# Kernel optimization log

Hardware: AMD Instinct MI355X
Metric: run time of the kernel (lower is better)

The kernel has to match this reference:

```python
import jax, jax.numpy as jnp
import numpy as np

B, N, D = 512, 100000, 64
TAU = 1e-4            # gumbel-softmax temperature from source
SIM_RATIO = 0.5       # similarity_ratio init kwarg
COS_EPS = 1e-6


def setup_inputs() -> dict:
    key = jax.random.key(0)
    k1, k2, k3, k4, k5 = jax.random.split(key, 5)
    need_replace = jax.random.randint(k1, (B, 2), 0, N, dtype=jnp.int64) if jax.config.jax_enable_x64 else jax.random.randint(k1, (B, 2), 0, N, dtype=jnp.int32)
    union_feature = jax.random.normal(k2, (B, 2 * D), dtype=jnp.float32)
    all_items = jax.random.normal(k3, (N, D), dtype=jnp.float32) * 0.1
    W = jax.random.normal(k4, (D, 2 * D), dtype=jnp.float32) * 0.05
    b = jax.random.normal(k5, (D,), dtype=jnp.float32) * 0.01
    return {"need_replace": need_replace, "union_feature": union_feature,
            "all_items": all_items, "W": W, "b": b}


def _cosine(a, b):
    # torch.nn.CosineSimilarity(dim=1, eps=1e-6): dot / max(||a||*||b||, eps)
    dot = jnp.sum(a * b, axis=1)
    na = jnp.linalg.norm(a, axis=1)
    nb = jnp.linalg.norm(b, axis=1)
    return dot / jnp.maximum(na * nb, COS_EPS)


def reference(need_replace, union_feature, all_items, W, b):
    item_ids = need_replace[:, 1]
    items_emb = all_items[item_ids]                      # [B, D]
    uif = union_feature @ W.T + b                        # [B, D] (nn.Linear)
    score = uif @ all_items.T                            # [B, N]

    # gumbel_softmax(tau=1e-4, hard=True), training branch
    g = jax.random.gumbel(jax.random.key(42), score.shape, dtype=score.dtype)
    y_soft = jax.nn.softmax((score + g) / TAU, axis=-1)  # [B, N]
    idx = jnp.argmax(y_soft, axis=-1)                    # [B]
    y_hard = jax.nn.one_hot(idx, N, dtype=score.dtype)
    P = y_hard + y_soft - jax.lax.stop_gradient(y_soft)  # straight-through hard one-hot

    item_sequence = jnp.arange(N, dtype=score.dtype)[None, :]
    replaceable_items = jnp.sum(P * item_sequence, axis=-1).astype(jnp.int32)
    replaceable_feat = P @ all_items                     # [B, D]

    sim = _cosine(items_emb, replaceable_feat)
    sim = (sim + 1.0) / 2.0                              # regularize_similarity
    labels = jnp.full((B,), SIM_RATIO, dtype=sim.dtype)
    similarity_loss = jnp.mean((sim - labels) ** 2)      # SimilarityMarginLoss (assumed MSE-to-margin)
    return replaceable_items, replaceable_feat, similarity_loss, jnp.mean(sim)
```

## Files before the change

### kernel.cpp

```cpp
#include <hip/hip_runtime.h>
#include <cstdint>

#define NITEMS   100000
#define BROWS    512
#define DDIM     64
#define S_BLOCKS 391
#define AM4_N    (S_BLOCKS * 4)
#define SB_OUT   256
#define NTILES   3125
#define FB_X     64
#define FB_Y     8
#define FB_CHUNK 1568
#define OUT_FEAT 512
#define OUT_LOSS (512 + 512 * 64)
#define OUT_MSIM (OUT_LOSS + 1)

#define BITS_RAW_T 4284334592u
#define G_TE       6.001f

typedef __attribute__((ext_vector_type(8)))  short  bf16x8;
typedef __attribute__((ext_vector_type(16))) float  f32x16;
typedef unsigned long long u64;
typedef uint32_t u32;

#define ROTL(x, r) __builtin_amdgcn_alignbit((x), (x), 32u - (r))

__device__ __forceinline__ u32 threefry_0_42_xor(u32 e) {
    const u32 K1 = 42u;
    const u32 K2 = 0x1BD11BDAu ^ 42u;
    u32 x0 = 0u;
    u32 x1 = e + K1;
#define TFR(r) { x0 += x1; x1 = ROTL(x1, r) ^ x0; }
    TFR(13u) TFR(15u) TFR(26u) TFR(6u)
    x0 += K1;  x1 += K2 + 1u;
    TFR(17u) TFR(29u) TFR(16u) TFR(24u)
    x0 += K2;  x1 += 2u;
    TFR(13u) TFR(15u) TFR(26u) TFR(6u)
    x1 += K1 + 3u;
    TFR(17u) TFR(29u) TFR(16u) TFR(24u)
    x0 += K1;  x1 += K2 + 4u;
    TFR(13u) TFR(15u) TFR(26u) TFR(6u)
    x0 += K2;  x1 += 5u;
#undef TFR
    return x0 ^ x1;
}

__device__ __forceinline__ void threefry_quad(u32 e0, u32 e1, u32 e2, u32 e3,
                                              u32& r0, u32& r1, u32& r2, u32& r3) {
    const u32 K1 = 42u;
    const u32 K2 = 0x1BD11BDAu ^ 42u;
    u32 a0 = 0u, a1 = e0 + K1;
    u32 b0 = 0u, b1 = e1 + K1;
    u32 c0 = 0u, c1 = e2 + K1;
    u32 d0 = 0u, d1 = e3 + K1;
#define TFR4(r) { a0 += a1; b0 += b1; c0 += c1; d0 += d1; \
                  a1 = ROTL(a1, r) ^ a0; b1 = ROTL(b1, r) ^ b0; \
                  c1 = ROTL(c1, r) ^ c0; d1 = ROTL(d1, r) ^ d0; }
    TFR4(13u) TFR4(15u) TFR4(26u) TFR4(6u)
    a0 += K1; a1 += K2 + 1u;  b0 += K1; b1 += K2 + 1u;
    c0 += K1; c1 += K2 + 1u;  d0 += K1; d1 += K2 + 1u;
    TFR4(17u) TFR4(29u) TFR4(16u) TFR4(24u)
    a0 += K2; a1 += 2u;       b0 += K2; b1 += 2u;
    c0 += K2; c1 += 2u;       d0 += K2; d1 += 2u;
    TFR4(13u) TFR4(15u) TFR4(26u) TFR4(6u)
    a1 += K1 + 3u;            b1 += K1 + 3u;
    c1 += K1 + 3u;            d1 += K1 + 3u;
    TFR4(17u) TFR4(29u) TFR4(16u) TFR4(24u)
    a0 += K1; a1 += K2 + 4u;  b0 += K1; b1 += K2 + 4u;
    c0 += K1; c1 += K2 + 4u;  d0 += K1; d1 += K2 + 4u;
    TFR4(13u) TFR4(15u) TFR4(26u) TFR4(6u)
    a0 += K2; a1 += 5u;       b0 += K2; b1 += 5u;
    c0 += K2; c1 += 5u;       d0 += K2; d1 += 5u;
#undef TFR4
    r0 = a0 ^ a1; r1 = b0 ^ b1; r2 = c0 ^ c1; r3 = d0 ^ d1;
}

__device__ __forceinline__ float gumbel_from_bits(u32 b) {
    float f = __uint_as_float((b >> 9) | 0x3F800000u) - 1.0f;
    f = fmaxf(f, 1.17549435e-38f);
    return -logf(-logf(f));
}
__device__ __forceinline__ u32 order_map(float v) {
    u32 x = __float_as_uint(v);
    return (x & 0x80000000u) ? ~x : (x | 0x80000000u);
}
__device__ __forceinline__ float unpack_val(u64 p) {
    u32 x = (u32)(p >> 32);
    u32 f = (x & 0x80000000u) ? (x & 0x7FFFFFFFu) : ~x;
    return __uint_as_float(f);
}
__device__ __forceinline__ short f32_to_bf16_rne(float f) {
    u32 b = __float_as_uint(f);
    u32 r = (b + 0x7FFFu + ((b >> 16) & 1u)) >> 16;
    return (short)r;
}
__device__ __forceinline__ float bf16_to_f32(short h) {
    return __uint_as_float(((u32)(uint16_t)h) << 16);
}

__global__ void prep_kernel(const float* __restrict__ UF, const float* __restrict__ W,
                            const float* __restrict__ bias, const float* __restrict__ A,
                            float* __restrict__ uif, float* __restrict__ unorm,
                            float* __restrict__ wsAM4, int* __restrict__ cnt,
                            int* __restrict__ done, float* __restrict__ out) {
    const int t = threadIdx.x, b = blockIdx.x;
    if (b == 0) {
        if (t == 0) { *cnt = 0; out[OUT_LOSS] = 0.f; out[OUT_MSIM] = 0.f; }
        done[t] = 0; done[t + 256] = 0;
    }
    if (b < 128) {
        __shared__ float Wt[128 * 65];
        for (int i = t; i < 8192; i += 256) {
            int d = i >> 7, k = i & 127;
            Wt[k * 65 + d] = W[i];
        }
        __syncthreads();
        const int row = b * 4 + (t >> 6);
        const int d   = t & 63;
        const float* u = UF + row * 128;
        float s = 0.f;
#pragma unroll 4
        for (int k = 0; k < 128; k++) s = fmaf(u[k], Wt[k * 65 + d], s);
        s += bias[d];
        uif[row * 64 + d] = s;
        float q = s * s;
#pragma unroll
        for (int o = 32; o >= 1; o >>= 1) q += __shfl_xor(q, o);
        if (d == 0) unorm[row] = sqrtf(q);
    } else {
        const int item = (b - 128) * 256 + t;
        float q = 0.f;
        if (item < NITEMS) {
            const float4* r = (const float4*)(A + (size_t)item * DDIM);
#pragma unroll
            for (int k = 0; k < 16; k++) {
                float4 x = r[k];
                q = fmaf(x.x, x.x, q); q = fmaf(x.y, x.y, q);
                q = fmaf(x.z, x.z, q); q = fmaf(x.w, x.w, q);
            }
        }
        float n = sqrtf(q);
#pragma unroll
        for (int o = 32; o >= 1; o >>= 1) n = fmaxf(n, __shfl_xor(n, o));
        if ((t & 63) == 0) wsAM4[(b - 128) * 4 + (t >> 6)] = n;
    }
}

__global__ __launch_bounds__(256, 6) void phase1_kernel(
        const float* __restrict__ A, const float* __restrict__ uif,
        u64* __restrict__ wsT1, float* __restrict__ wsB) {
    __shared__ bf16x8 sh_ah[4 * 64];
    __shared__ bf16x8 sh_al[4 * 64];
    const int tid  = threadIdx.x;
    const int lane = tid & 63;
    const int wv   = tid >> 6;
    const int rg   = blockIdx.y;
    const int xb   = blockIdx.x;
    const int row   = rg * 128 + wv * 32 + (lane & 31);
    const int khalf = (lane >> 5) * 8;

    bf16x8 uh[4], ul[4];
#pragma unroll
    for (int s = 0; s < 4; s++) {
        const float* src = uif + row * 64 + khalf + 16 * s;
        float4 v0 = *(const float4*)src;
        float4 v1 = *(const float4*)(src + 4);
        float vv[8] = {v0.x, v0.y, v0.z, v0.w, v1.x, v1.y, v1.z, v1.w};
        bf16x8 h, l2;
#pragma unroll
        for (int j = 0; j < 8; j++) {
            short hh = f32_to_bf16_rne(vv[j]);
            float r  = vv[j] - bf16_to_f32(hh);
            h[j] = hh; l2[j] = f32_to_bf16_rne(r);
        }
        uh[s] = h; ul[s] = l2;
    }

    u64 t1p = 0ull; float t1f = -3.0e38f, t2f = -3.0e38f, sm = -3.0e38f;
    const u32 rowbase_e = (u32)row * (u32)NITEMS;

    const int s_i   = tid & 31;
    const int s_c   = tid >> 5;
    const int s_dst = (s_c >> 1) * 64 + s_i + 32 * (s_c & 1);
    const float* s_srcbase = A + (size_t)s_i * 64 + 8 * s_c;

    int t_idx = xb;
    float4 p0 = *(const float4*)(s_srcbase + (size_t)t_idx * (32 * 64));
    float4 p1 = *(const float4*)(s_srcbase + (size_t)t_idx * (32 * 64) + 4);

    while (t_idx < NTILES) {
        const int tb = t_idx * 32;
        bf16x8 h, l2;
        {
            float vv[8] = {p0.x, p0.y, p0.z, p0.w, p1.x, p1.y, p1.z, p1.w};
#pragma unroll
            for (int j = 0; j < 8; j++) {
                short hh = f32_to_bf16_rne(vv[j]);
                float r  = vv[j] - bf16_to_f32(hh);
                h[j] = hh; l2[j] = f32_to_bf16_rne(r);
            }
        }
        __syncthreads();
        sh_ah[s_dst] = h; sh_al[s_dst] = l2;
        __syncthreads();
        t_idx += SB_OUT;
        if (t_idx < NTILES) {
            const float* src = s_srcbase + (size_t)t_idx * (32 * 64);
            p0 = *(const float4*)src;
            p1 = *(const float4*)(src + 4);
        }

        f32x16 acc;
#pragma unroll
        for (int z = 0; z < 16; z++) acc[z] = 0.0f;
#pragma unroll
        for (int s = 0; s < 4; s++) {
            bf16x8 ah = sh_ah[s * 64 + lane];
            bf16x8 al = sh_al[s * 64 + lane];
            acc = __builtin_amdgcn_mfma_f32_32x32x16_bf16(ah, uh[s], acc, 0, 0, 0);
            acc = __builtin_amdgcn_mfma_f32_32x32x16_bf16(al, uh[s], acc, 0, 0, 0);
            acc = __builtin_amdgcn_mfma_f32_32x32x16_bf16(ah, ul[s], acc, 0, 0, 0);
        }

        const int ib4 = tb + 4 * (lane >> 5);
#pragma unroll
        for (int i = 0; i < 16; i += 4) {
            const int i0 = ib4 + 2 * i;
            u32 r0, r1, r2, r3;
            threefry_quad(rowbase_e + (u32)(i0 + 0), rowbase_e + (u32)(i0 + 1),
                          rowbase_e + (u32)(i0 + 2), rowbase_e + (u32)(i0 + 3),
                          r0, r1, r2, r3);
            float sA = acc[i], sB = acc[i + 1], sC = acc[i + 2], sD = acc[i + 3];
            sm = fmaxf(sm, fmaxf(fmaxf(sA, sB), fmaxf(sC, sD)));
            if (r0 >= BITS_RAW_T) {
                float v = sA + gumbel_from_bits(r0);
                if (v > t1f) {
                    t2f = t1f; t1f = v;
                    t1p = ((u64)order_map(v) << 32) | (u32)(~(u32)(i0 + 0));
                } else t2f = fmaxf(t2f, v);
            }
            if (r1 >= BITS_RAW_T) {
                float v = sB + gumbel_from_bits(r1);
                if (v > t1f) {
                    t2f = t1f; t1f = v;
                    t1p = ((u64)order_map(v) << 32) | (u32)(~(u32)(i0 + 1));
                } else t2f = fmaxf(t2f, v);
            }
            if (r2 >= BITS_RAW_T) {
                float v = sC + gumbel_from_bits(r2);
                if (v > t1f) {
                    t2f = t1f; t1f = v;
                    t1p = ((u64)order_map(v) << 32) | (u32)(~(u32)(i0 + 2));
                } else t2f = fmaxf(t2f, v);
            }
            if (r3 >= BITS_RAW_T) {
                float v = sD + gumbel_from_bits(r3);
                if (v > t1f) {
                    t2f = t1f; t1f = v;
                    t1p = ((u64)order_map(v) << 32) | (u32)(~(u32)(i0 + 3));
                } else t2f = fmaxf(t2f, v);
            }
        }
    }

    float bnd = fmaxf(t2f, sm + G_TE);
    {
        u64   op = __shfl_xor(t1p, 32);
        float of = __shfl_xor(t1f, 32);
        float ob = __shfl_xor(bnd, 32);
        if (op > t1p) { bnd = fmaxf(fmaxf(bnd, ob), t1f); t1p = op; t1f = of; }
        else          { bnd = fmaxf(fmaxf(bnd, ob), of); }
    }
    if (lane < 32) {
        wsT1[(size_t)row * SB_OUT + xb] = t1p;
        wsB [(size_t)row * SB_OUT + xb] = bnd;
    }
}

__global__ void merge_kernel(const u64* __restrict__ wsT1, const float* __restrict__ wsB,
                             const float* __restrict__ wsAM4, const float* __restrict__ unorm,
                             const float* __restrict__ A, const int* __restrict__ need_replace,
                             u64* __restrict__ packed, int* __restrict__ rowlist,
                             int* __restrict__ cnt, float* __restrict__ out) {
    const int row = blockIdx.x, t = threadIdx.x;
    float am = 0.f;
    for (int i = t; i < AM4_N; i += 64) am = fmaxf(am, wsAM4[i]);
    u64 p1 = 0ull; float f1 = -3.0e38f, f2 = -3.0e38f;
    for (int sbk = t; sbk < SB_OUT; sbk += 64) {
        u64   ep = wsT1[(size_t)row * SB_OUT + sbk];
        float e2 = wsB [(size_t)row * SB_OUT + sbk];
        if (ep > p1) { f2 = fmaxf(fmaxf(f1, e2), f2); p1 = ep; f1 = unpack_val(ep); }
        else         { float v = unpack_val(ep); f2 = fmaxf(f2, fmaxf(v, e2)); }
    }
#pragma unroll
    for (int off = 1; off < 64; off <<= 1) {
        u64   op  = __shfl_xor(p1, off);
        float of1 = __shfl_xor(f1, off);
        float of2 = __shfl_xor(f2, off);
        am = fmaxf(am, __shfl_xor(am, off));
        if (op > p1) { f2 = fmaxf(fmaxf(f1, of2), f2); p1 = op; f1 = of1; }
        else         { f2 = fmaxf(f2, fmaxf(of1, of2)); }
    }
    const float E = 1.5e-4f * unorm[row] * am + 3.0e-5f;
    if (f1 - f2 > 2.0f * E) {
        const int idx = (int)(~(u32)(p1 & 0xFFFFFFFFull));
        float fr = A[(size_t)idx * DDIM + t];
        out[OUT_FEAT + row * DDIM + t] = fr;
        int   item = need_replace[2 * row + 1];
        float fa   = A[(size_t)item * DDIM + t];
        float dot = fa * fr, na2 = fa * fa, nb2 = fr * fr;
#pragma unroll
        for (int o = 32; o >= 1; o >>= 1) {
            dot += __shfl_down(dot, o);
            na2 += __shfl_down(na2, o);
            nb2 += __shfl_down(nb2, o);
        }
        if (t == 0) {
            out[row] = (float)idx;
            float denom = fmaxf(sqrtf(na2) * sqrtf(nb2), 1e-6f);
            float sim = (dot / denom + 1.0f) * 0.5f;
            float d = sim - 0.5f;
            atomicAdd(&out[OUT_LOSS], d * d * (1.0f / 512.0f));
            atomicAdd(&out[OUT_MSIM], sim * (1.0f / 512.0f));
        }
    } else if (t == 0) {
        packed[row] = 0ull;
        rowlist[atomicAdd(cnt, 1)] = row;
    }
}

__global__ void fallback_kernel(const float* __restrict__ A, const float* __restrict__ uif,
                                const int* __restrict__ rowlist, const int* __restrict__ cnt,
                                const int* __restrict__ need_replace,
                                u64* __restrict__ packed, int* __restrict__ done,
                                float* __restrict__ out) {
    __shared__ float Us[64];
    __shared__ int   sh_last;
    const int t  = threadIdx.x;
    const int xb = blockIdx.x;
    const int total = *cnt;
    const int iend = min((xb + 1) * FB_CHUNK, NITEMS);

    for (int li = blockIdx.y; li < total; li += FB_Y) {
        const int row = rowlist[li];
        __syncthreads();
        if (t < 64) Us[t] = uif[row * 64 + t];
        __syncthreads();
        u64 pk = 0ull;
        for (int item = xb * FB_CHUNK + t; item < iend; item += 256) {
            u32 rb  = threefry_0_42_xor((u32)row * (u32)NITEMS + (u32)item);
            float g = gumbel_from_bits(rb);
            const float4* a4 = (const float4*)(A + (size_t)item * DDIM);
            float s0 = 0.f, s1 = 0.f;
#pragma unroll
            for (int k = 0; k < 16; k += 2) {
                float4 x = a4[k];
                float4 y = a4[k + 1];
                s0 = fmaf(x.x, Us[4*k    ], s0);
                s0 = fmaf(x.y, Us[4*k + 1], s0);
                s0 = fmaf(x.z, Us[4*k + 2], s0);
                s0 = fmaf(x.w, Us[4*k + 3], s0);
                s1 = fmaf(y.x, Us[4*k + 4], s1);
                s1 = fmaf(y.y, Us[4*k + 5], s1);
                s1 = fmaf(y.z, Us[4*k + 6], s1);
                s1 = fmaf(y.w, Us[4*k + 7], s1);
            }
            float v = (s0 + s1) + g;
            u64 c = ((u64)order_map(v) << 32) | (u32)(~(u32)item);
            pk = (c > pk) ? c : pk;
        }
#pragma unroll
        for (int off = 1; off < 64; off <<= 1) {
            u64 o = __shfl_xor(pk, off);
            pk = (o > pk) ? o : pk;
        }
        if ((t & 63) == 0) atomicMax(&packed[row], pk);
        __syncthreads();
        if (t == 0) {
            __threadfence();
            sh_last = (atomicAdd(&done[li], 1) == FB_X - 1) ? 1 : 0;
        }
        __syncthreads();
        if (sh_last && t < 64) {
            u64 fin = atomicMax(&packed[row], 0ull);
            const int idx = (int)(~(u32)(fin & 0xFFFFFFFFull));
            float fr = A[(size_t)idx * DDIM + t];
            out[OUT_FEAT + row * DDIM + t] = fr;
            int   item = need_replace[2 * row + 1];
            float fa   = A[(size_t)item * DDIM + t];
            float dot = fa * fr, na2 = fa * fa, nb2 = fr * fr;
#pragma unroll
            for (int o = 32; o >= 1; o >>= 1) {
                dot += __shfl_down(dot, o);
                na2 += __shfl_down(na2, o);
                nb2 += __shfl_down(nb2, o);
            }
            if (t == 0) {
                out[row] = (float)idx;
                float denom = fmaxf(sqrtf(na2) * sqrtf(nb2), 1e-6f);
                float sim = (dot / denom + 1.0f) * 0.5f;
                float d = sim - 0.5f;
                atomicAdd(&out[OUT_LOSS], d * d * (1.0f / 512.0f));
                atomicAdd(&out[OUT_MSIM], sim * (1.0f / 512.0f));
            }
        }
        __syncthreads();
    }
}

extern "C" void kernel_launch(void* const* d_in, const int* in_sizes, int n_in,
                              void* d_out, int out_size, void* d_ws, size_t ws_size,
                              hipStream_t stream) {
    (void)in_sizes; (void)n_in; (void)out_size; (void)ws_size;
    const int*   need_replace = (const int*)d_in[0];
    const float* UF           = (const float*)d_in[1];
    const float* A            = (const float*)d_in[2];
    const float* W            = (const float*)d_in[3];
    const float* bias         = (const float*)d_in[4];
    float* out = (float*)d_out;

    char* ws = (char*)d_ws;
    u64*   wsT1    = (u64*)  (ws);
    float* wsB     = (float*)(ws + 1048576);
    float* uif     = (float*)(ws + 1572864);
    u64*   packed  = (u64*)  (ws + 1703936);
    float* unorm   = (float*)(ws + 1708032);
    float* wsAM4   = (float*)(ws + 1710080);
    int*   rowlist = (int*)  (ws + 1716336);
    int*   cnt     = (int*)  (ws + 1718384);
    int*   done    = (int*)  (ws + 1718388);

    prep_kernel<<<519, 256, 0, stream>>>(UF, W, bias, A, uif, unorm, wsAM4, cnt, done, out);
    phase1_kernel<<<dim3(SB_OUT, 4), 256, 0, stream>>>(A, uif, wsT1, wsB);
    merge_kernel<<<BROWS, 64, 0, stream>>>(wsT1, wsB, wsAM4, unorm, A, need_replace,
                                           packed, rowlist, cnt, out);
    fallback_kernel<<<dim3(FB_X, FB_Y), 256, 0, stream>>>(A, uif, rowlist, cnt,
                                                          need_replace, packed, done, out);
}
```

Before: 251.3 us.

## Double-buffer phase1 tiles, use atomic work-stealing, and defer gumbel candidate processing

Phase1 now takes tiles from a per-row-group atomic counter instead of a fixed stride, and double-buffers the bf16 split tiles in LDS so conversion of the next tile overlaps the MFMAs with one barrier per tile. Gumbel candidates that pass the threshold are pushed into a per-wave LDS queue rather than updating top-1/top-2 inline. The queue is reduced after the loop with shared atomics. Queue overflow forces a conservative bound so rows fall to the fallback path. This trades divergent per-element branching for LDS atomics and extra shared memory, which may lower occupancy.

```diff
diff --git a/kernel.cpp b/kernel.cpp
--- a/kernel.cpp
+++ b/kernel.cpp
@@ -8,6 +8,7 @@
 #define AM4_N    (S_BLOCKS * 4)
 #define SB_OUT   256
 #define NTILES   3125
+#define QCAP     192
 #define FB_X     64
 #define FB_Y     8
 #define FB_CHUNK 1568
@@ -97,15 +98,27 @@
 __device__ __forceinline__ float bf16_to_f32(short h) {
     return __uint_as_float(((u32)(uint16_t)h) << 16);
 }
+__device__ __forceinline__ void conv_split(const float4& p0, const float4& p1,
+                                           bf16x8& h, bf16x8& l2) {
+    float vv[8] = {p0.x, p0.y, p0.z, p0.w, p1.x, p1.y, p1.z, p1.w};
+#pragma unroll
+    for (int j = 0; j < 8; j++) {
+        short hh = f32_to_bf16_rne(vv[j]);
+        float r  = vv[j] - bf16_to_f32(hh);
+        h[j] = hh; l2[j] = f32_to_bf16_rne(r);
+    }
+}
 
 __global__ void prep_kernel(const float* __restrict__ UF, const float* __restrict__ W,
                             const float* __restrict__ bias, const float* __restrict__ A,
                             float* __restrict__ uif, float* __restrict__ unorm,
                             float* __restrict__ wsAM4, int* __restrict__ cnt,
-                            int* __restrict__ done, float* __restrict__ out) {
+                            int* __restrict__ done, int* __restrict__ tctr,
+                            float* __restrict__ out) {
     const int t = threadIdx.x, b = blockIdx.x;
     if (b == 0) {
         if (t == 0) { *cnt = 0; out[OUT_LOSS] = 0.f; out[OUT_MSIM] = 0.f; }
+        if (t < 4) tctr[t] = 0;
         done[t] = 0; done[t + 256] = 0;
     }
     if (b < 128) {
@@ -148,16 +161,25 @@
 
 __global__ __launch_bounds__(256, 6) void phase1_kernel(
         const float* __restrict__ A, const float* __restrict__ uif,
-        u64* __restrict__ wsT1, float* __restrict__ wsB) {
-    __shared__ bf16x8 sh_ah[4 * 64];
-    __shared__ bf16x8 sh_al[4 * 64];
+        int* __restrict__ tctr, u64* __restrict__ wsT1, float* __restrict__ wsB) {
+    __shared__ bf16x8 sh_ah[2][4 * 64];
+    __shared__ bf16x8 sh_al[2][4 * 64];
+    __shared__ u64 qsb[4][QCAP];
+    __shared__ u32 qmeta[4][QCAP];
+    __shared__ u32 qcnt[4];
+    __shared__ u64 t1tab[4][32];
+    __shared__ u32 t2tab[4][32];
+    __shared__ int sh_t[2];
+
     const int tid  = threadIdx.x;
     const int lane = tid & 63;
     const int wv   = tid >> 6;
     const int rg   = blockIdx.y;
     const int xb   = blockIdx.x;
     const int row   = rg * 128 + wv * 32 + (lane & 31);
+    const u32 lrow  = (u32)(lane & 31);
     const int khalf = (lane >> 5) * 8;
+    int* ctr = tctr + rg;
 
     bf16x8 uh[4], ul[4];
 #pragma unroll
@@ -165,18 +187,10 @@
         const float* src = uif + row * 64 + khalf + 16 * s;
         float4 v0 = *(const float4*)src;
         float4 v1 = *(const float4*)(src + 4);
-        float vv[8] = {v0.x, v0.y, v0.z, v0.w, v1.x, v1.y, v1.z, v1.w};
-        bf16x8 h, l2;
-#pragma unroll
-        for (int j = 0; j < 8; j++) {
-            short hh = f32_to_bf16_rne(vv[j]);
-            float r  = vv[j] - bf16_to_f32(hh);
-            h[j] = hh; l2[j] = f32_to_bf16_rne(r);
-        }
-        uh[s] = h; ul[s] = l2;
-    }
-
-    u64 t1p = 0ull; float t1f = -3.0e38f, t2f = -3.0e38f, sm = -3.0e38f;
+        conv_split(v0, v1, uh[s], ul[s]);
+    }
+
+    float sm = -3.0e38f;
     const u32 rowbase_e = (u32)row * (u32)NITEMS;
 
     const int s_i   = tid & 31;
@@ -184,44 +198,47 @@
     const int s_dst = (s_c >> 1) * 64 + s_i + 32 * (s_c & 1);
     const float* s_srcbase = A + (size_t)s_i * 64 + 8 * s_c;
 
-    int t_idx = xb;
-    float4 p0 = *(const float4*)(s_srcbase + (size_t)t_idx * (32 * 64));
-    float4 p1 = *(const float4*)(s_srcbase + (size_t)t_idx * (32 * 64) + 4);
-
-    while (t_idx < NTILES) {
-        const int tb = t_idx * 32;
+    if (tid < 4) qcnt[tid] = 0;
+    if (tid == 0) sh_t[0] = atomicAdd(ctr, 1);
+    __syncthreads();
+    int t_cur = sh_t[0];
+    float4 p0, p1;
+    if (t_cur < NTILES) {
+        const float* src = s_srcbase + (size_t)t_cur * 2048;
+        p0 = *(const float4*)src;
+        p1 = *(const float4*)(src + 4);
+    }
+    if (tid == 0) sh_t[1] = atomicAdd(ctr, 1);
+    if (t_cur < NTILES) {
         bf16x8 h, l2;
-        {
-            float vv[8] = {p0.x, p0.y, p0.z, p0.w, p1.x, p1.y, p1.z, p1.w};
-#pragma unroll
-            for (int j = 0; j < 8; j++) {
-                short hh = f32_to_bf16_rne(vv[j]);
-                float r  = vv[j] - bf16_to_f32(hh);
-                h[j] = hh; l2[j] = f32_to_bf16_rne(r);
-            }
-        }
-        __syncthreads();
-        sh_ah[s_dst] = h; sh_al[s_dst] = l2;
-        __syncthreads();
-        t_idx += SB_OUT;
-        if (t_idx < NTILES) {
-            const float* src = s_srcbase + (size_t)t_idx * (32 * 64);
+        conv_split(p0, p1, h, l2);
+        sh_ah[0][s_dst] = h; sh_al[0][s_dst] = l2;
+    }
+    __syncthreads();
+    int t_next = sh_t[1];
+    int tog = 0;
+
+    while (t_cur < NTILES) {
+        if (t_next < NTILES) {
+            const float* src = s_srcbase + (size_t)t_next * 2048;
             p0 = *(const float4*)src;
             p1 = *(const float4*)(src + 4);
         }
+        if (tid == 0) sh_t[tog] = atomicAdd(ctr, 1);
 
         f32x16 acc;
 #pragma unroll
         for (int z = 0; z < 16; z++) acc[z] = 0.0f;
 #pragma unroll
         for (int s = 0; s < 4; s++) {
-            bf16x8 ah = sh_ah[s * 64 + lane];
-            bf16x8 al = sh_al[s * 64 + lane];
+            bf16x8 ah = sh_ah[tog][s * 64 + lane];
+            bf16x8 al = sh_al[tog][s * 64 + lane];
             acc = __builtin_amdgcn_mfma_f32_32x32x16_bf16(ah, uh[s], acc, 0, 0, 0);
             acc = __builtin_amdgcn_mfma_f32_32x32x16_bf16(al, uh[s], acc, 0, 0, 0);
             acc = __builtin_amdgcn_mfma_f32_32x32x16_bf16(ah, ul[s], acc, 0, 0, 0);
         }
 
+        const int tb  = t_cur * 32;
         const int ib4 = tb + 4 * (lane >> 5);
 #pragma unroll
         for (int i = 0; i < 16; i += 4) {
@@ -233,45 +250,77 @@
             float sA = acc[i], sB = acc[i + 1], sC = acc[i + 2], sD = acc[i + 3];
             sm = fmaxf(sm, fmaxf(fmaxf(sA, sB), fmaxf(sC, sD)));
             if (r0 >= BITS_RAW_T) {
-                float v = sA + gumbel_from_bits(r0);
-                if (v > t1f) {
-                    t2f = t1f; t1f = v;
-                    t1p = ((u64)order_map(v) << 32) | (u32)(~(u32)(i0 + 0));
-                } else t2f = fmaxf(t2f, v);
+                u32 qi = atomicAdd(&qcnt[wv], 1u);
+                if (qi < QCAP) {
+                    qsb[wv][qi]   = ((u64)__float_as_uint(sA) << 32) | r0;
+                    qmeta[wv][qi] = (u32)(i0 + 0) | (lrow << 17);
+                }
             }
             if (r1 >= BITS_RAW_T) {
-                float v = sB + gumbel_from_bits(r1);
-                if (v > t1f) {
-                    t2f = t1f; t1f = v;
-                    t1p = ((u64)order_map(v) << 32) | (u32)(~(u32)(i0 + 1));
-                } else t2f = fmaxf(t2f, v);
+                u32 qi = atomicAdd(&qcnt[wv], 1u);
+                if (qi < QCAP) {
+                    qsb[wv][qi]   = ((u64)__float_as_uint(sB) << 32) | r1;
+                    qmeta[wv][qi] = (u32)(i0 + 1) | (lrow << 17);
+                }
             }
             if (r2 >= BITS_RAW_T) {
-                float v = sC + gumbel_from_bits(r2);
-                if (v > t1f) {
-                    t2f = t1f; t1f = v;
-                    t1p = ((u64)order_map(v) << 32) | (u32)(~(u32)(i0 + 2));
-                } else t2f = fmaxf(t2f, v);
+                u32 qi = atomicAdd(&qcnt[wv], 1u);
+                if (qi < QCAP) {
+                    qsb[wv][qi]   = ((u64)__float_as_uint(sC) << 32) | r2;
+                    qmeta[wv][qi] = (u32)(i0 + 2) | (lrow << 17);
+                }
             }
             if (r3 >= BITS_RAW_T) {
-                float v = sD + gumbel_from_bits(r3);
-                if (v > t1f) {
-                    t2f = t1f; t1f = v;
-                    t1p = ((u64)order_map(v) << 32) | (u32)(~(u32)(i0 + 3));
-                } else t2f = fmaxf(t2f, v);
-            }
-        }
-    }
-
-    float bnd = fmaxf(t2f, sm + G_TE);
-    {
-        u64   op = __shfl_xor(t1p, 32);
-        float of = __shfl_xor(t1f, 32);
-        float ob = __shfl_xor(bnd, 32);
-        if (op > t1p) { bnd = fmaxf(fmaxf(bnd, ob), t1f); t1p = op; t1f = of; }
-        else          { bnd = fmaxf(fmaxf(bnd, ob), of); }
-    }
+                u32 qi = atomicAdd(&qcnt[wv], 1u);
+                if (qi < QCAP) {
+                    qsb[wv][qi]   = ((u64)__float_as_uint(sD) << 32) | r3;
+                    qmeta[wv][qi] = (u32)(i0 + 3) | (lrow << 17);
+                }
+            }
+        }
+
+        if (t_next < NTILES) {
+            bf16x8 h, l2;
+            conv_split(p0, p1, h, l2);
+            sh_ah[tog ^ 1][s_dst] = h; sh_al[tog ^ 1][s_dst] = l2;
+        }
+        __syncthreads();
+        t_cur = t_next;
+        t_next = sh_t[tog];
+        tog ^= 1;
+    }
+
+    const u32 nq = qcnt[wv];
+    if (lane < 32) { t1tab[wv][lane] = 0ull; t2tab[wv][lane] = 0u; }
+    __syncthreads();
+    const int n = (int)(nq < (u32)QCAP ? nq : (u32)QCAP);
+    for (int i = lane; i < n; i += 64) {
+        u64 sb   = qsb[wv][i];
+        u32 meta = qmeta[wv][i];
+        float sc = __uint_as_float((u32)(sb >> 32));
+        float v  = sc + gumbel_from_bits((u32)sb);
+        u32 item = meta & 0x1FFFFu;
+        u32 r    = meta >> 17;
+        u64 pk   = ((u64)order_map(v) << 32) | (u32)(~item);
+        qsb[wv][i] = pk;
+        atomicMax((unsigned long long*)&t1tab[wv][r], (unsigned long long)pk);
+    }
+    __syncthreads();
+    for (int i = lane; i < n; i += 64) {
+        u64 pk = qsb[wv][i];
+        u32 r  = qmeta[wv][i] >> 17;
+        if (pk != t1tab[wv][r]) {
+            u32 vb = (u32)(pk >> 32) & 0x7FFFFFFFu;
+            atomicMax(&t2tab[wv][r], vb);
+        }
+    }
+    __syncthreads();
+    sm = fmaxf(sm, __shfl_xor(sm, 32));
     if (lane < 32) {
+        u64   t1p = t1tab[wv][lane];
+        float t2v = __uint_as_float(t2tab[wv][lane]);
+        if (nq > (u32)QCAP) t2v = 3.0e38f;
+        float bnd = fmaxf(t2v, sm + G_TE);
         wsT1[(size_t)row * SB_OUT + xb] = t1p;
         wsB [(size_t)row * SB_OUT + xb] = bnd;
     }
@@ -429,9 +478,11 @@
     int*   rowlist = (int*)  (ws + 1716336);
     int*   cnt     = (int*)  (ws + 1718384);
     int*   done    = (int*)  (ws + 1718388);
-
-    prep_kernel<<<519, 256, 0, stream>>>(UF, W, bias, A, uif, unorm, wsAM4, cnt, done, out);
-    phase1_kernel<<<dim3(SB_OUT, 4), 256, 0, stream>>>(A, uif, wsT1, wsB);
+    int*   tctr    = (int*)  (ws + 1720436);
+
+    prep_kernel<<<519, 256, 0, stream>>>(UF, W, bias, A, uif, unorm, wsAM4, cnt, done,
+                                         tctr, out);
+    phase1_kernel<<<dim3(SB_OUT, 4), 256, 0, stream>>>(A, uif, tctr, wsT1, wsB);
     merge_kernel<<<BROWS, 64, 0, stream>>>(wsT1, wsB, wsAM4, unorm, A, need_replace,
                                            packed, rowlist, cnt, out);
     fallback_kernel<<<dim3(FB_X, FB_Y), 256, 0, stream>>>(A, uif, rowlist, cnt,
```

Result: slower. 275.6 us (+9.7%).
